# Performance work log

Measured on AMD Instinct MI355X. Metric: run time of the kernel, lower is better.

## Reference

```python
import jax, jax.numpy as jnp
import numpy as np

PLANE_RES = 1024
FEAT_DIM = 2
LEVELS = 4
# scales = ceil(128*2^i - 1)+1 = [128, 256, 512, 1024]; plane_res/scale is exactly [8,4,2,1]
SCALES = np.array([128.0, 256.0, 512.0, 1024.0], dtype=np.float32)
FACTORS = np.array([8, 4, 2, 1], dtype=np.int32)


def setup_inputs() -> dict:
    key = jax.random.key(0)
    k1, k2 = jax.random.split(key)
    B = 2097152
    positions = jax.random.uniform(k1, (B, 3), dtype=jnp.float32)  # points in [0,1)
    table_size = PLANE_RES * PLANE_RES * 3 * FEAT_DIM
    plane_embedding = jax.random.normal(k2, (table_size,), dtype=jnp.float32) * 1e-2
    return {"positions": positions, "plane_embedding": plane_embedding}


def _encode(positions, plane_embedding):
    B = positions.shape[0]
    scales = jnp.asarray(SCALES)            # (L,)
    factors = jnp.asarray(FACTORS)          # (L,) int32, = plane_res/scale exactly
    # pos = xyz*(scale-1)+0.5 per level -> (B, L, 3)
    pos = positions[:, None, :] * (scales[None, :, None] - 1.0) + 0.5
    grid = jnp.floor(pos).astype(jnp.int32)
    frac = pos - grid
    # plane coordinate pairs: xy=(x,y), yz=(y,z), zx=(z,x)
    c0 = jnp.array([0, 1, 2])
    c1 = jnp.array([1, 2, 0])
    f0, f1 = frac[..., c0], frac[..., c1]   # (B, L, 3)
    g0, g1 = grid[..., c0], grid[..., c1]   # (B, L, 3)
    tab = plane_embedding.reshape(3, PLANE_RES * PLANE_RES, FEAT_DIM)
    plane_idx = jnp.arange(3)[None, None, :]
    fac = factors[None, :, None]
    acc = jnp.zeros((B, LEVELS, 3, FEAT_DIM), dtype=positions.dtype)
    for dx in (0, 1):  # static 4-corner bilinear loop
        wx = f0 if dx else (1.0 - f0)
        i0 = jnp.minimum((g0 + dx) * fac, PLANE_RES - 1)
        for dy in (0, 1):
            wy = f1 if dy else (1.0 - f1)
            i1 = jnp.minimum((g1 + dy) * fac, PLANE_RES - 1)
            idx = i0 + i1 * PLANE_RES           # (B, L, 3) flat index in each plane
            feats = tab[plane_idx, idx]          # (B, L, 3, F) irregular gather
            acc = acc + (wx * wy)[..., None] * feats
    prod = acc[..., 0, :] * acc[..., 1, :] * acc[..., 2, :]  # (B, L, F)
    out = jnp.concatenate([acc, prod[..., None, :]], axis=2)  # (B, L, 4, F)
    # layout: level*8 + plane_slot*2 + j, matching the Taichi output indexing
    return out.reshape(B, LEVELS * 4 * FEAT_DIM)


def reference(positions, plane_embedding):
    return _encode(positions, plane_embedding)
```

## Files before the change

### kernel.cpp

```cpp
#include <hip/hip_runtime.h>

#define PLANE_RES 1024
#define PLANE_STRIDE (PLANE_RES * PLANE_RES)
#define NBUCKETS 32768
#define SCAN_THREADS 1024
#define PER_THREAD (NBUCKETS / SCAN_THREADS)

__device__ __forceinline__ void encode_one(
    float x, float y, float z, const float2* __restrict__ tab, float* res)
{
    const float scales[4] = {128.0f, 256.0f, 512.0f, 1024.0f};
    const int   facs[4]   = {8, 4, 2, 1};

    #pragma unroll
    for (int l = 0; l < 4; ++l) {
        const float s = scales[l] - 1.0f;
        const float px = x * s + 0.5f;
        const float py = y * s + 0.5f;
        const float pz = z * s + 0.5f;
        const int gx = (int)floorf(px);
        const int gy = (int)floorf(py);
        const int gz = (int)floorf(pz);
        const float fx = px - (float)gx;
        const float fy = py - (float)gy;
        const float fz = pz - (float)gz;
        const int fac = facs[l];

        const int   g0s[3] = {gx, gy, gz};
        const int   g1s[3] = {gy, gz, gx};
        const float f0s[3] = {fx, fy, fz};
        const float f1s[3] = {fy, fz, fx};

        float acc[3][2];

        #pragma unroll
        for (int p = 0; p < 3; ++p) {
            const int i0a = min(g0s[p] * fac,       PLANE_RES - 1);
            const int i0b = min((g0s[p] + 1) * fac, PLANE_RES - 1);
            const int i1a = min(g1s[p] * fac,       PLANE_RES - 1);
            const int i1b = min((g1s[p] + 1) * fac, PLANE_RES - 1);

            const float2* __restrict__ base = tab + (size_t)p * PLANE_STRIDE;
            const float2 c00 = base[i0a + i1a * PLANE_RES];
            const float2 c01 = base[i0a + i1b * PLANE_RES];
            const float2 c10 = base[i0b + i1a * PLANE_RES];
            const float2 c11 = base[i0b + i1b * PLANE_RES];

            const float w0 = f0s[p], w1 = f1s[p];
            float a0 = (1.0f - w0) * (1.0f - w1) * c00.x;
            float a1 = (1.0f - w0) * (1.0f - w1) * c00.y;
            a0 += (1.0f - w0) * w1 * c01.x;
            a1 += (1.0f - w0) * w1 * c01.y;
            a0 += w0 * (1.0f - w1) * c10.x;
            a1 += w0 * (1.0f - w1) * c10.y;
            a0 += w0 * w1 * c11.x;
            a1 += w0 * w1 * c11.y;
            acc[p][0] = a0;
            acc[p][1] = a1;
        }

        res[l * 8 + 0] = acc[0][0];
        res[l * 8 + 1] = acc[0][1];
        res[l * 8 + 2] = acc[1][0];
        res[l * 8 + 3] = acc[1][1];
        res[l * 8 + 4] = acc[2][0];
        res[l * 8 + 5] = acc[2][1];
        res[l * 8 + 6] = acc[0][0] * acc[1][0] * acc[2][0];
        res[l * 8 + 7] = acc[0][1] * acc[1][1] * acc[2][1];
    }
}

__device__ __forceinline__ unsigned part1by2(unsigned v) {
    v &= 0x3ff;
    v = (v | (v << 16)) & 0x030000FFu;
    v = (v | (v << 8))  & 0x0300F00Fu;
    v = (v | (v << 4))  & 0x030C30C3u;
    v = (v | (v << 2))  & 0x09249249u;
    return v;
}

__device__ __forceinline__ unsigned morton_key(float x, float y, float z) {
    int gx = (int)floorf(x * 1023.0f + 0.5f);
    int gy = (int)floorf(y * 1023.0f + 0.5f);
    int gz = (int)floorf(z * 1023.0f + 0.5f);
    unsigned bx = ((unsigned)gx) >> 5;
    unsigned by = ((unsigned)gy) >> 5;
    unsigned bz = ((unsigned)gz) >> 5;
    return (part1by2(bx) << 2) | (part1by2(by) << 1) | part1by2(bz);
}

__global__ __launch_bounds__(256) void hist_kernel(
    const float* __restrict__ positions, unsigned* __restrict__ hist, int B)
{
    int i = blockIdx.x * blockDim.x + threadIdx.x;
    if (i >= B) return;
    const float x = positions[(size_t)i * 3 + 0];
    const float y = positions[(size_t)i * 3 + 1];
    const float z = positions[(size_t)i * 3 + 2];
    atomicAdd(&hist[morton_key(x, y, z)], 1u);
}

__global__ __launch_bounds__(SCAN_THREADS) void scan_kernel(unsigned* __restrict__ hist)
{
    __shared__ unsigned partials[SCAN_THREADS];
    const int t = threadIdx.x;
    unsigned vals[PER_THREAD];
    unsigned sum = 0;
    #pragma unroll
    for (int j = 0; j < PER_THREAD; ++j) {
        vals[j] = hist[t * PER_THREAD + j];
        sum += vals[j];
    }
    partials[t] = sum;
    __syncthreads();
    #pragma unroll
    for (int off = 1; off < SCAN_THREADS; off <<= 1) {
        unsigned u = (t >= off) ? partials[t - off] : 0u;
        __syncthreads();
        partials[t] += u;
        __syncthreads();
    }
    unsigned running = partials[t] - sum;
    #pragma unroll
    for (int j = 0; j < PER_THREAD; ++j) {
        unsigned v = vals[j];
        hist[t * PER_THREAD + j] = running;
        running += v;
    }
}

__global__ __launch_bounds__(256) void scatter_kernel(
    const float* __restrict__ positions, unsigned* __restrict__ offs,
    float4* __restrict__ sorted, int B)
{
    int i = blockIdx.x * blockDim.x + threadIdx.x;
    if (i >= B) return;
    const float x = positions[(size_t)i * 3 + 0];
    const float y = positions[(size_t)i * 3 + 1];
    const float z = positions[(size_t)i * 3 + 2];
    unsigned k = morton_key(x, y, z);
    unsigned dst = atomicAdd(&offs[k], 1u);
    sorted[dst] = make_float4(x, y, z, __int_as_float(i));
}

__global__ __launch_bounds__(256) void triplane_sorted_kernel(
    const float4* __restrict__ sorted,
    const float* __restrict__ plane_embedding,
    float* __restrict__ out, int B, int swizzle)
{
    int b = blockIdx.x;
    if (swizzle) {
        int per = gridDim.x >> 3;
        b = (b & 7) * per + (b >> 3);
    }
    int i = b * blockDim.x + threadIdx.x;
    if (i >= B) return;

    const float4 p = sorted[i];
    const int orig = __float_as_int(p.w);
    const float2* __restrict__ tab = (const float2*)plane_embedding;

    float res[32];
    encode_one(p.x, p.y, p.z, tab, res);

    float4* __restrict__ o4 = (float4*)(out + (size_t)orig * 32);
    #pragma unroll
    for (int j = 0; j < 8; ++j) {
        o4[j] = make_float4(res[j * 4 + 0], res[j * 4 + 1],
                            res[j * 4 + 2], res[j * 4 + 3]);
    }
}

__global__ __launch_bounds__(256) void triplane_plain_kernel(
    const float* __restrict__ positions,
    const float* __restrict__ plane_embedding,
    float* __restrict__ out, int B)
{
    int i = blockIdx.x * blockDim.x + threadIdx.x;
    if (i >= B) return;
    const float x = positions[(size_t)i * 3 + 0];
    const float y = positions[(size_t)i * 3 + 1];
    const float z = positions[(size_t)i * 3 + 2];
    const float2* __restrict__ tab = (const float2*)plane_embedding;
    float res[32];
    encode_one(x, y, z, tab, res);
    float4* __restrict__ o4 = (float4*)(out + (size_t)i * 32);
    #pragma unroll
    for (int j = 0; j < 8; ++j) {
        o4[j] = make_float4(res[j * 4 + 0], res[j * 4 + 1],
                            res[j * 4 + 2], res[j * 4 + 3]);
    }
}

extern "C" void kernel_launch(void* const* d_in, const int* in_sizes, int n_in,
                              void* d_out, int out_size, void* d_ws, size_t ws_size,
                              hipStream_t stream) {
    const float* positions = (const float*)d_in[0];
    const float* plane_embedding = (const float*)d_in[1];
    float* out = (float*)d_out;
    const int B = in_sizes[0] / 3;

    const int block = 256;
    const int grid = (B + block - 1) / block;

    const size_t offs_bytes = (size_t)NBUCKETS * sizeof(unsigned);
    const size_t need = offs_bytes + (size_t)B * sizeof(float4);

    if (ws_size < need) {
        triplane_plain_kernel<<<grid, block, 0, stream>>>(positions, plane_embedding, out, B);
        return;
    }

    unsigned* offs = (unsigned*)d_ws;
    float4* sorted = (float4*)((char*)d_ws + offs_bytes);

    hipMemsetAsync(offs, 0, offs_bytes, stream);
    hist_kernel<<<grid, block, 0, stream>>>(positions, offs, B);
    scan_kernel<<<1, SCAN_THREADS, 0, stream>>>(offs);
    scatter_kernel<<<grid, block, 0, stream>>>(positions, offs, sorted, B);

    const int swizzle = (grid % 8 == 0) ? 1 : 0;
    triplane_sorted_kernel<<<grid, block, 0, stream>>>(sorted, plane_embedding, out, B, swizzle);
}
```

Baseline: 740.4 us.

## Split per-point encoding across four threads, one per level, with nontemporal stores

The sorted triplane kernel now maps each 64-point wave group onto four waves, one per resolution level, so each thread does 12 gathers instead of 48. All gather addresses are computed before the loads are issued, which exposes more memory-level parallelism and lowers register pressure per thread. Output is written as two nontemporal 16-byte stores per thread, meant to avoid polluting cache with the write stream. In exchange, every thread reloads the sorted position, and the grid grows fourfold.

```diff
diff --git a/kernel.cpp b/kernel.cpp
--- a/kernel.cpp
+++ b/kernel.cpp
@@ -5,6 +5,8 @@
 #define NBUCKETS 32768
 #define SCAN_THREADS 1024
 #define PER_THREAD (NBUCKETS / SCAN_THREADS)
+
+typedef float nfloat4 __attribute__((ext_vector_type(4)));
 
 __device__ __forceinline__ void encode_one(
     float x, float y, float z, const float2* __restrict__ tab, float* res)
@@ -143,7 +145,7 @@
     sorted[dst] = make_float4(x, y, z, __int_as_float(i));
 }
 
-__global__ __launch_bounds__(256) void triplane_sorted_kernel(
+__global__ __launch_bounds__(256) void triplane_lvl_kernel(
     const float4* __restrict__ sorted,
     const float* __restrict__ plane_embedding,
     float* __restrict__ out, int B, int swizzle)
@@ -153,22 +155,78 @@
         int per = gridDim.x >> 3;
         b = (b & 7) * per + (b >> 3);
     }
-    int i = b * blockDim.x + threadIdx.x;
+    const int lane  = threadIdx.x & 63;
+    const int level = threadIdx.x >> 6;
+    const int i = b * 64 + lane;
     if (i >= B) return;
 
     const float4 p = sorted[i];
     const int orig = __float_as_int(p.w);
     const float2* __restrict__ tab = (const float2*)plane_embedding;
 
-    float res[32];
-    encode_one(p.x, p.y, p.z, tab, res);
-
-    float4* __restrict__ o4 = (float4*)(out + (size_t)orig * 32);
-    #pragma unroll
-    for (int j = 0; j < 8; ++j) {
-        o4[j] = make_float4(res[j * 4 + 0], res[j * 4 + 1],
-                            res[j * 4 + 2], res[j * 4 + 3]);
-    }
+    const int   fac = 8 >> level;
+    const float s   = (float)(128 << level) - 1.0f;
+
+    const float px = p.x * s + 0.5f;
+    const float py = p.y * s + 0.5f;
+    const float pz = p.z * s + 0.5f;
+    const int gx = (int)floorf(px);
+    const int gy = (int)floorf(py);
+    const int gz = (int)floorf(pz);
+    const float fx = px - (float)gx;
+    const float fy = py - (float)gy;
+    const float fz = pz - (float)gz;
+
+    const int   g0s[3] = {gx, gy, gz};
+    const int   g1s[3] = {gy, gz, gx};
+    const float f0s[3] = {fx, fy, fz};
+    const float f1s[3] = {fy, fz, fx};
+
+    int off[3][4];
+    #pragma unroll
+    for (int pl = 0; pl < 3; ++pl) {
+        const int i0a = min(g0s[pl] * fac,       PLANE_RES - 1);
+        const int i0b = min((g0s[pl] + 1) * fac, PLANE_RES - 1);
+        const int r1a = min(g1s[pl] * fac,       PLANE_RES - 1) * PLANE_RES;
+        const int r1b = min((g1s[pl] + 1) * fac, PLANE_RES - 1) * PLANE_RES;
+        off[pl][0] = i0a + r1a;
+        off[pl][1] = i0a + r1b;
+        off[pl][2] = i0b + r1a;
+        off[pl][3] = i0b + r1b;
+    }
+
+    float2 c[3][4];
+    #pragma unroll
+    for (int pl = 0; pl < 3; ++pl) {
+        const float2* __restrict__ base = tab + (size_t)pl * PLANE_STRIDE;
+        #pragma unroll
+        for (int k = 0; k < 4; ++k) {
+            c[pl][k] = base[off[pl][k]];
+        }
+    }
+
+    float acc[3][2];
+    #pragma unroll
+    for (int pl = 0; pl < 3; ++pl) {
+        const float w0 = f0s[pl], w1 = f1s[pl];
+        const float w00 = (1.0f - w0) * (1.0f - w1);
+        const float w01 = (1.0f - w0) * w1;
+        const float w10 = w0 * (1.0f - w1);
+        const float w11 = w0 * w1;
+        acc[pl][0] = w00 * c[pl][0].x + w01 * c[pl][1].x
+                   + w10 * c[pl][2].x + w11 * c[pl][3].x;
+        acc[pl][1] = w00 * c[pl][0].y + w01 * c[pl][1].y
+                   + w10 * c[pl][2].y + w11 * c[pl][3].y;
+    }
+
+    nfloat4 o0 = { acc[0][0], acc[0][1], acc[1][0], acc[1][1] };
+    nfloat4 o1 = { acc[2][0], acc[2][1],
+                   acc[0][0] * acc[1][0] * acc[2][0],
+                   acc[0][1] * acc[1][1] * acc[2][1] };
+
+    nfloat4* __restrict__ o4 = (nfloat4*)(out + (size_t)orig * 32 + level * 8);
+    __builtin_nontemporal_store(o0, o4);
+    __builtin_nontemporal_store(o1, o4 + 1);
 }
 
 __global__ __launch_bounds__(256) void triplane_plain_kernel(
@@ -214,11 +272,12 @@
     unsigned* offs = (unsigned*)d_ws;
     float4* sorted = (float4*)((char*)d_ws + offs_bytes);
 
-    hipMemsetAsync(offs, 0, offs_bytes, stream);
+    (void)hipMemsetAsync(offs, 0, offs_bytes, stream);
     hist_kernel<<<grid, block, 0, stream>>>(positions, offs, B);
     scan_kernel<<<1, SCAN_THREADS, 0, stream>>>(offs);
     scatter_kernel<<<grid, block, 0, stream>>>(positions, offs, sorted, B);
 
-    const int swizzle = (grid % 8 == 0) ? 1 : 0;
-    triplane_sorted_kernel<<<grid, block, 0, stream>>>(sorted, plane_embedding, out, B, swizzle);
-}
+    const int mgrid = (B + 63) / 64;
+    const int swizzle = (mgrid % 8 == 0) ? 1 : 0;
+    triplane_lvl_kernel<<<mgrid, block, 0, stream>>>(sorted, plane_embedding, out, B, swizzle);
+}
```

Measured after the change: 1.082 ms. 1.46x slower.
